# Performance work log

Hardware: AMD Instinct MI355X
Metric: run time of the kernel (lower is better)

Reference implementation:

```python
import jax, jax.numpy as jnp
import numpy as np
import math

D_MODEL = 512
N_HEADS = 16
HEAD_DIM = D_MODEL // N_HEADS  # 32
ROPE_BASE = 10000.0
B, T = 2, 2048


def build_rope_cache(seq_len, dim, base):
    inv_freq = 1.0 / (base ** (jnp.arange(0, dim, 2, dtype=jnp.float32) / dim))  # (dim/2,)
    t = jnp.arange(seq_len, dtype=jnp.float32)
    freqs = jnp.outer(t, inv_freq)                  # (T, dim/2)
    emb = jnp.concatenate([freqs, freqs], axis=-1)  # (T, dim)
    return jnp.cos(emb), jnp.sin(emb)


def rotate_half(x):
    x1, x2 = jnp.split(x, 2, axis=-1)
    return jnp.concatenate([-x2, x1], axis=-1)


def apply_rope(x, cos, sin):
    # x: (B,H,T,hd); cos/sin: (T,hd) broadcast over B,H
    return x * cos + rotate_half(x) * sin


def setup_inputs() -> dict:
    key = jax.random.key(0)
    k1, k2, k3 = jax.random.split(key, 3)
    x = jax.random.normal(k1, (B, T, D_MODEL), dtype=jnp.float32)
    w_qkv = jax.random.normal(k2, (3 * D_MODEL, D_MODEL), dtype=jnp.float32) * 0.02
    w_o = jax.random.normal(k3, (D_MODEL, D_MODEL), dtype=jnp.float32) * 0.02
    return {"x": x, "w_qkv": w_qkv, "w_o": w_o}


def reference(x, w_qkv, w_o):
    Bx, Tx, C = x.shape
    H, hd = N_HEADS, HEAD_DIM
    qkv = x @ w_qkv.T                                   # (B,T,3C)
    qkv = qkv.reshape(Bx, Tx, 3, H, hd).transpose(0, 2, 3, 1, 4)  # (B,3,H,T,hd)
    q, k, v = qkv[:, 0], qkv[:, 1], qkv[:, 2]
    cos, sin = build_rope_cache(Tx, hd, ROPE_BASE)
    q = apply_rope(q, cos, sin)
    k = apply_rope(k, cos, sin)
    scale = 1.0 / math.sqrt(hd)
    scores = jnp.einsum('bhqd,bhkd->bhqk', q, k) * scale  # (B,H,T,T)
    causal = jnp.tril(jnp.ones((Tx, Tx), dtype=bool))
    scores = jnp.where(causal, scores, jnp.finfo(scores.dtype).min)
    attn = jax.nn.softmax(scores, axis=-1)
    out = jnp.einsum('bhqk,bhkd->bhqd', attn, v)          # (B,H,T,hd)
    out = out.transpose(0, 2, 1, 3).reshape(Bx, Tx, C)    # (B,T,C)
    return out @ w_o.T
```

## Files before the change

kernel.cpp:

```cpp
#include <hip/hip_runtime.h>
#include <hip/hip_bf16.h>
#include <math.h>

#define D_MODEL 512
#define N_HEADS 16
#define HEAD_DIM 32
#define T_SEQ 2048
#define B_SZ 2
#define NTOK (B_SZ * T_SEQ)
#define QKV_DIM (3 * D_MODEL)

#define LOG2_10000_D16 0.8304820237218405f
#define QSCALE_LOG2 0.2550348788f
#define NROPE (T_SEQ * 16)

typedef short short8 __attribute__((ext_vector_type(8)));
typedef float f32x4  __attribute__((ext_vector_type(4)));

__device__ __forceinline__ float bf2f(unsigned int u16) {
    union { unsigned int i; float f; } v;
    v.i = u16 << 16;
    return v.f;
}

__device__ __forceinline__ unsigned short f2bf(float f) {
    union { float f; unsigned int i; } v;
    v.f = f;
    unsigned int lsb = (v.i >> 16) & 1u;
    v.i += 0x7fffu + lsb;
    return (unsigned short)(v.i >> 16);
}

__device__ __forceinline__ unsigned short f2bf_trunc(float f) {
    union { float f; unsigned int i; } v;
    v.f = f;
    return (unsigned short)(v.i >> 16);
}

__device__ __forceinline__ void gld_lds16(const void* g, void* l) {
    __builtin_amdgcn_global_load_lds(
        (const __attribute__((address_space(1))) void*)g,
        (__attribute__((address_space(3))) void*)l, 16, 0, 0);
}

#define N4_X   (NTOK * D_MODEL / 4)
#define N4_WQ  (QKV_DIM * D_MODEL / 4)
#define N4_WO  (D_MODEL * D_MODEL / 4)
__global__ __launch_bounds__(256) void cvt_all(const float* __restrict__ x,
                                               const float* __restrict__ wq,
                                               const float* __restrict__ wo,
                                               unsigned short* __restrict__ xb,
                                               unsigned short* __restrict__ wqb,
                                               unsigned short* __restrict__ wob,
                                               float2* __restrict__ rope) {
    int i = blockIdx.x * 256 + threadIdx.x;
    if (i >= N4_X + N4_WQ + N4_WO) {
        int kk = i - (N4_X + N4_WQ + N4_WO);
        if (kk < NROPE) {
            int t = kk >> 4, cd = kk & 15;
            float invf = exp2f(-LOG2_10000_D16 * (float)cd);
            float ss, cc;
            sincosf((float)t * invf, &ss, &cc);
            rope[kk] = make_float2(cc, ss);
        }
        return;
    }
    const float* in;
    unsigned short* out;
    int k;
    if (i < N4_X)                { in = x;  out = xb;  k = i; }
    else if (i < N4_X + N4_WQ)   { in = wq; out = wqb; k = i - N4_X; }
    else                         { in = wo; out = wob; k = i - N4_X - N4_WQ; }
    float4 v = ((const float4*)in)[k];
    ushort4 o;
    o.x = f2bf(v.x); o.y = f2bf(v.y); o.z = f2bf(v.z); o.w = f2bf(v.w);
    ((ushort4*)out)[k] = o;
}

template<int MT, int LDA, int LDC, bool OUT_BF16, bool ROPE>
__global__ __launch_bounds__(256) void gemm_nt(const unsigned short* __restrict__ A,
                                               const unsigned short* __restrict__ B,
                                               void* __restrict__ Cout,
                                               unsigned short* __restrict__ kb,
                                               unsigned short* __restrict__ vt,
                                               const float2* __restrict__ rope) {
    __shared__ unsigned short Als[MT * 64];
    __shared__ unsigned short Bls[64 * 64];

    const int tid = threadIdx.x;
    const int m0 = blockIdx.y * MT;
    const int n0 = blockIdx.x * 64;

    const int wid  = tid >> 6;
    const int lane = tid & 63;
    const int c    = lane & 15;
    const int quad = lane >> 4;
    const int wm = (wid >> 1) * (MT / 2);
    const int wn = (wid & 1) * 32;
    const int MI = MT / 32;

    f32x4 acc[MI][2];
#pragma unroll
    for (int i = 0; i < MI; ++i)
#pragma unroll
        for (int j = 0; j < 2; ++j) acc[i][j] = (f32x4)0.f;

    const int srow = wid * 8 + (lane >> 3);
    const int schk = lane & 7;

    for (int k0 = 0; k0 < 512; k0 += 64) {
#pragma unroll
        for (int it = 0; it < MT / 32; ++it) {
            const unsigned short* g = A + (size_t)(m0 + it * 32 + srow) * LDA + k0 + schk * 8;
            gld_lds16(g, &Als[(it * 32 + srow) * 64 + schk * 8]);
        }
#pragma unroll
        for (int it = 0; it < 2; ++it) {
            const unsigned short* g = B + (size_t)(n0 + it * 32 + srow) * 512 + k0 + schk * 8;
            gld_lds16(g, &Bls[(it * 32 + srow) * 64 + schk * 8]);
        }
        __syncthreads();

#pragma unroll
        for (int kk = 0; kk < 2; ++kk) {
            short8 af[MI], bfr[2];
#pragma unroll
            for (int i = 0; i < MI; ++i)
                af[i] = *(const short8*)&Als[(wm + i * 16 + c) * 64 + kk * 32 + quad * 8];
#pragma unroll
            for (int j = 0; j < 2; ++j)
                bfr[j] = *(const short8*)&Bls[(wn + j * 16 + c) * 64 + kk * 32 + quad * 8];
#pragma unroll
            for (int i = 0; i < MI; ++i)
#pragma unroll
                for (int j = 0; j < 2; ++j)
                    acc[i][j] = __builtin_amdgcn_mfma_f32_16x16x32_bf16(af[i], bfr[j], acc[i][j], 0, 0, 0);
        }
        __syncthreads();
    }

    if (ROPE) {
        const int sec = n0 >> 9;
        if (sec == 0) {
            const float2* rp = rope + c;
#pragma unroll
            for (int i = 0; i < MI; ++i)
#pragma unroll
                for (int r = 0; r < 4; ++r) {
                    int t = (m0 + wm + i * 16 + quad * 4 + r) & (T_SEQ - 1);
                    float2 cs = rp[t * 16];
                    float e0 = acc[i][0][r], e1 = acc[i][1][r];
                    acc[i][0][r] = (e0 * cs.x - e1 * cs.y) * QSCALE_LOG2;
                    acc[i][1][r] = (e1 * cs.x + e0 * cs.y) * QSCALE_LOG2;
                }
        } else if (sec == 1) {
            const float2* rp = rope + c;
            const int head = ((n0 - 512) + wn) >> 5;
#pragma unroll
            for (int i = 0; i < MI; ++i)
#pragma unroll
                for (int r = 0; r < 4; ++r) {
                    int mm = m0 + wm + i * 16 + quad * 4 + r;
                    int t = mm & (T_SEQ - 1);
                    float2 cs = rp[t * 16];
                    float e0 = acc[i][0][r], e1 = acc[i][1][r];
                    float k0v = e0 * cs.x - e1 * cs.y;
                    float k1v = e1 * cs.x + e0 * cs.y;
                    int bh = (mm >> 11) * 16 + head;
                    int s = (t & 3) ^ ((t >> 2) & 3);
                    unsigned short* row = kb + ((size_t)(bh * 2048 + t)) * 32;
                    row[((((c) >> 3) ^ s) << 3) + (c & 7)]        = f2bf(k0v);
                    row[((((16 + c) >> 3) ^ s) << 3) + (c & 7)]   = f2bf(k1v);
                }
            return;
        } else {
#pragma unroll
            for (int i = 0; i < MI; ++i)
#pragma unroll
                for (int j = 0; j < 2; ++j) {
                    int nl = n0 - 1024 + wn + j * 16;
                    int head = nl >> 5;
                    int d = (nl & 16) + c;
                    int mm = m0 + wm + i * 16 + quad * 4;
                    int bI = mm >> 11;
                    int pos = mm & (T_SEQ - 1);
                    int phys = ((pos >> 3) & 7) ^ (d & 7);
                    size_t base = ((size_t)((bI * 16 + head) * 32 + d)) * 2048
                                  + (pos & ~63) + (phys << 3) + (pos & 7);
                    ushort4 st;
                    st.x = f2bf(acc[i][j][0]); st.y = f2bf(acc[i][j][1]);
                    st.z = f2bf(acc[i][j][2]); st.w = f2bf(acc[i][j][3]);
                    *(ushort4*)(vt + base) = st;
                }
            return;
        }
    }

    if (OUT_BF16) {
        unsigned short* Cb = (unsigned short*)Cout;
#pragma unroll
        for (int i = 0; i < MI; ++i)
#pragma unroll
            for (int j = 0; j < 2; ++j)
#pragma unroll
                for (int r = 0; r < 4; ++r) {
                    int mm = m0 + wm + i * 16 + quad * 4 + r;
                    int nn = n0 + wn + j * 16 + c;
                    Cb[(size_t)mm * LDC + nn] = f2bf(acc[i][j][r]);
                }
    } else {
        float* Cf = (float*)Cout;
#pragma unroll
        for (int i = 0; i < MI; ++i)
#pragma unroll
            for (int j = 0; j < 2; ++j)
#pragma unroll
                for (int r = 0; r < 4; ++r) {
                    int mm = m0 + wm + i * 16 + quad * 4 + r;
                    int nn = n0 + wn + j * 16 + c;
                    Cf[(size_t)mm * LDC + nn] = acc[i][j][r];
                }
    }
}

__global__ __launch_bounds__(256) void flash_attn(unsigned short* __restrict__ qb,
                                                  const unsigned short* __restrict__ kb,
                                                  const unsigned short* __restrict__ vt) {
    __shared__ unsigned short KtL[2][64 * 32];
    __shared__ unsigned short VtL[2][32 * 64];
    __shared__ unsigned short Pl[4 * 16 * 64];

    const int idx   = blockIdx.x;
    const int qtile = 31 - (idx >> 5);
    const int bh    = idx & 31;
    const int b = bh >> 4, h = bh & 15;
    const int tid  = threadIdx.x;
    const int wid  = tid >> 6;
    const int lane = tid & 63;
    const int c    = lane & 15;
    const int quad = lane >> 4;

    const int q0w = qtile * 64 + wid * 16;
    const int sK = (c & 3) ^ ((c >> 2) & 3);
    const int sP = c & 7;

    short8 qf = *(const short8*)(qb + ((size_t)(b * T_SEQ + q0w + c)) * 512 + h * HEAD_DIM + quad * 8);

    f32x4 accO[2];
    accO[0] = (f32x4)0.f; accO[1] = (f32x4)0.f;
    float l_r[4] = {0.f, 0.f, 0.f, 0.f};

    unsigned short* plw = &Pl[wid * 16 * 64];

    const int krow = tid >> 2, kch = tid & 3;
    const int vd   = tid >> 3, vch = tid & 7;
    const unsigned short* kbase = kb + (size_t)bh * 2048 * 32 + (size_t)krow * 32 + kch * 8;
    const unsigned short* vbase = vt + ((size_t)(bh * 32 + vd)) * 2048 + vch * 8;

    uint4 kreg = *(const uint4*)(kbase);
    uint4 vreg = *(const uint4*)(vbase);
    *(uint4*)&KtL[0][tid * 8] = kreg;
    *(uint4*)&VtL[0][tid * 8] = vreg;
    __syncthreads();

    const int nkt = qtile + 1;
    for (int kt = 0; kt < nkt; ++kt) {
        const int cur = kt & 1;
        const bool pf_next = (kt + 1 < nkt);
        if (pf_next) {
            kreg = *(const uint4*)(kbase + (size_t)(kt + 1) * 64 * 32);
            vreg = *(const uint4*)(vbase + (size_t)(kt + 1) * 64);
        }

        f32x4 sv[4];
        __builtin_amdgcn_s_setprio(1);
#pragma unroll
        for (int j = 0; j < 4; ++j) {
            short8 kf = *(const short8*)&KtL[cur][(j * 16 + c) * 32 + ((quad ^ sK) << 3)];
            f32x4 z = (f32x4)0.f;
            sv[j] = __builtin_amdgcn_mfma_f32_16x16x32_bf16(qf, kf, z, 0, 0, 0);
        }
        __builtin_amdgcn_s_setprio(0);

        if (kt == qtile) {
#pragma unroll
            for (int j = 0; j < 4; ++j)
#pragma unroll
                for (int r = 0; r < 4; ++r)
                    if (j * 16 + c > wid * 16 + quad * 4 + r) sv[j][r] = -30000.f;
        }

#pragma unroll
        for (int j = 0; j < 4; ++j)
#pragma unroll
            for (int r = 0; r < 4; ++r) {
                float p = exp2f(sv[j][r]);
                l_r[r] += p;
                int row = quad * 4 + r;
                plw[row * 64 + (((j * 2 + (c >> 3)) ^ (row & 7)) << 3) + (c & 7)] = f2bf_trunc(p);
            }

        __builtin_amdgcn_s_setprio(1);
#pragma unroll
        for (int kk = 0; kk < 2; ++kk) {
            short8 pf = *(const short8*)&plw[c * 64 + (((kk * 4 + quad) ^ sP) << 3)];
#pragma unroll
            for (int ns = 0; ns < 2; ++ns) {
                short8 vf = *(const short8*)&VtL[cur][(ns * 16 + c) * 64 + (((kk * 4 + quad) ^ sP) << 3)];
                accO[ns] = __builtin_amdgcn_mfma_f32_16x16x32_bf16(pf, vf, accO[ns], 0, 0, 0);
            }
        }
        __builtin_amdgcn_s_setprio(0);

        if (pf_next) {
            *(uint4*)&KtL[cur ^ 1][tid * 8] = kreg;
            *(uint4*)&VtL[cur ^ 1][tid * 8] = vreg;
        }
        __syncthreads();
    }

#pragma unroll
    for (int r = 0; r < 4; ++r) {
        float lr = l_r[r];
        lr += __shfl_xor(lr, 1);
        lr += __shfl_xor(lr, 2);
        lr += __shfl_xor(lr, 4);
        lr += __shfl_xor(lr, 8);
        float inv = 1.f / lr;
        int qg = q0w + quad * 4 + r;
        unsigned short* op = qb + ((size_t)(b * T_SEQ + qg)) * 512 + h * HEAD_DIM;
#pragma unroll
        for (int ns = 0; ns < 2; ++ns)
            op[ns * 16 + c] = f2bf(accO[ns][r] * inv);
    }
}

extern "C" void kernel_launch(void* const* d_in, const int* in_sizes, int n_in,
                              void* d_out, int out_size, void* d_ws, size_t ws_size,
                              hipStream_t stream) {
    const float* x     = (const float*)d_in[0];
    const float* w_qkv = (const float*)d_in[1];
    const float* w_o   = (const float*)d_in[2];
    float* out = (float*)d_out;

    unsigned short* qb  = (unsigned short*)d_ws;
    unsigned short* kb  = qb  + (size_t)NTOK * D_MODEL;
    unsigned short* vt  = kb  + (size_t)32 * 2048 * 32;
    unsigned short* xb  = vt  + (size_t)32 * 32 * 2048;
    unsigned short* wqb = xb  + (size_t)NTOK * D_MODEL;
    unsigned short* wob = wqb + (size_t)QKV_DIM * D_MODEL;
    float2*         rope = (float2*)(wob + (size_t)D_MODEL * D_MODEL);

    {
        int total = N4_X + N4_WQ + N4_WO + NROPE;
        cvt_all<<<(total + 255) / 256, 256, 0, stream>>>(x, w_qkv, w_o, xb, wqb, wob, rope);
    }
    {
        dim3 grid(QKV_DIM / 64, NTOK / 128);
        gemm_nt<128, D_MODEL, D_MODEL, true, true><<<grid, 256, 0, stream>>>(xb, wqb, qb, kb, vt, rope);
    }
    {
        flash_attn<<<1024, 256, 0, stream>>>(qb, kb, vt);
    }
    {
        dim3 grid(D_MODEL / 64, NTOK / 64);
        gemm_nt<64, D_MODEL, D_MODEL, false, false><<<grid, 256, 0, stream>>>(qb, wob, out, nullptr, nullptr, nullptr);
    }
}
```

Measured before the change: 124.1 us.

## Split long causal query tiles across two blocks and combine partial outputs

The 16 longest causal query tiles per head now have their key range split between two blocks, which write unnormalized partial outputs and row sums to workspace. A new combine kernel adds the two partials, normalizes them, and writes bf16 results. Short tiles still run in a single block and write their output directly. The aim is to shorten the critical path caused by the triangular imbalance of work across blocks. The cost is an extra kernel launch plus fp32 partial-result traffic. Summing partials without rescaling is only correct because the kernel appears not to subtract a per-row running max.

```diff
diff --git a/kernel.cpp b/kernel.cpp
--- a/kernel.cpp
+++ b/kernel.cpp
@@ -225,14 +225,34 @@
 
 __global__ __launch_bounds__(256) void flash_attn(unsigned short* __restrict__ qb,
                                                   const unsigned short* __restrict__ kb,
-                                                  const unsigned short* __restrict__ vt) {
+                                                  const unsigned short* __restrict__ vt,
+                                                  float* __restrict__ pO,
+                                                  float* __restrict__ pL) {
     __shared__ unsigned short KtL[2][64 * 32];
     __shared__ unsigned short VtL[2][32 * 64];
     __shared__ unsigned short Pl[4 * 16 * 64];
 
-    const int idx   = blockIdx.x;
-    const int qtile = 31 - (idx >> 5);
-    const int bh    = idx & 31;
+    const int blk = blockIdx.x;
+    const int g   = blk >> 5;
+    const int bh  = blk & 31;
+    int qtile, kt0, ktN, sidx;
+    bool partial;
+    if (g < 16) {
+        qtile = 31 - g;
+        int nkt = qtile + 1;
+        kt0 = 0; ktN = nkt >> 1;
+        partial = true; sidx = (qtile - 16) * 2;
+    } else if (g < 32) {
+        qtile = 31 - (g - 16);
+        int nkt = qtile + 1;
+        kt0 = nkt >> 1; ktN = nkt;
+        partial = true; sidx = (qtile - 16) * 2 + 1;
+    } else {
+        qtile = 15 - (g - 32);
+        kt0 = 0; ktN = qtile + 1;
+        partial = false; sidx = 0;
+    }
+
     const int b = bh >> 4, h = bh & 15;
     const int tid  = threadIdx.x;
     const int wid  = tid >> 6;
@@ -257,16 +277,15 @@
     const unsigned short* kbase = kb + (size_t)bh * 2048 * 32 + (size_t)krow * 32 + kch * 8;
     const unsigned short* vbase = vt + ((size_t)(bh * 32 + vd)) * 2048 + vch * 8;
 
-    uint4 kreg = *(const uint4*)(kbase);
-    uint4 vreg = *(const uint4*)(vbase);
+    uint4 kreg = *(const uint4*)(kbase + (size_t)kt0 * 64 * 32);
+    uint4 vreg = *(const uint4*)(vbase + (size_t)kt0 * 64);
     *(uint4*)&KtL[0][tid * 8] = kreg;
     *(uint4*)&VtL[0][tid * 8] = vreg;
     __syncthreads();
 
-    const int nkt = qtile + 1;
-    for (int kt = 0; kt < nkt; ++kt) {
-        const int cur = kt & 1;
-        const bool pf_next = (kt + 1 < nkt);
+    for (int kt = kt0; kt < ktN; ++kt) {
+        const int cur = (kt - kt0) & 1;
+        const bool pf_next = (kt + 1 < ktN);
         if (pf_next) {
             kreg = *(const uint4*)(kbase + (size_t)(kt + 1) * 64 * 32);
             vreg = *(const uint4*)(vbase + (size_t)(kt + 1) * 64);
@@ -326,13 +345,45 @@
         lr += __shfl_xor(lr, 2);
         lr += __shfl_xor(lr, 4);
         lr += __shfl_xor(lr, 8);
-        float inv = 1.f / lr;
-        int qg = q0w + quad * 4 + r;
-        unsigned short* op = qb + ((size_t)(b * T_SEQ + qg)) * 512 + h * HEAD_DIM;
-#pragma unroll
-        for (int ns = 0; ns < 2; ++ns)
-            op[ns * 16 + c] = f2bf(accO[ns][r] * inv);
-    }
+        int qrl = wid * 16 + quad * 4 + r;
+        if (partial) {
+            size_t rb = ((size_t)(bh * 32 + sidx)) * 64 + qrl;
+            if (c == 0) pL[rb] = lr;
+            pO[rb * 32 + c]      = accO[0][r];
+            pO[rb * 32 + 16 + c] = accO[1][r];
+        } else {
+            float inv = 1.f / lr;
+            int qg = qtile * 64 + qrl;
+            unsigned short* op = qb + ((size_t)(b * T_SEQ + qg)) * 512 + h * HEAD_DIM;
+#pragma unroll
+            for (int ns = 0; ns < 2; ++ns)
+                op[ns * 16 + c] = f2bf(accO[ns][r] * inv);
+        }
+    }
+}
+
+__global__ __launch_bounds__(256) void combine_split(const float* __restrict__ pO,
+                                                     const float* __restrict__ pL,
+                                                     unsigned short* __restrict__ qb) {
+    int idx = blockIdx.x * 256 + threadIdx.x;
+    int row = idx >> 3;
+    int dc  = (idx & 7) * 4;
+    int bh  = row >> 10;
+    int rem = row & 1023;
+    int qt16 = rem >> 6;
+    int qr  = rem & 63;
+    size_t slot0 = ((size_t)(bh * 32 + qt16 * 2)) * 64 + qr;
+    float4 a  = *(const float4*)(pO + slot0 * 32 + dc);
+    float4 bv = *(const float4*)(pO + (slot0 + 64) * 32 + dc);
+    float inv = 1.f / (pL[slot0] + pL[slot0 + 64]);
+    ushort4 o;
+    o.x = f2bf((a.x + bv.x) * inv);
+    o.y = f2bf((a.y + bv.y) * inv);
+    o.z = f2bf((a.z + bv.z) * inv);
+    o.w = f2bf((a.w + bv.w) * inv);
+    int t = (16 + qt16) * 64 + qr;
+    int b = bh >> 4, h = bh & 15;
+    *(ushort4*)(qb + ((size_t)(b * T_SEQ + t)) * 512 + h * HEAD_DIM + dc) = o;
 }
 
 extern "C" void kernel_launch(void* const* d_in, const int* in_sizes, int n_in,
@@ -350,6 +401,8 @@
     unsigned short* wqb = xb  + (size_t)NTOK * D_MODEL;
     unsigned short* wob = wqb + (size_t)QKV_DIM * D_MODEL;
     float2*         rope = (float2*)(wob + (size_t)D_MODEL * D_MODEL);
+    float*          pO   = (float*)(rope + NROPE);
+    float*          pL   = pO + (size_t)32 * 32 * 64 * 32;
 
     {
         int total = N4_X + N4_WQ + N4_WO + NROPE;
@@ -360,7 +413,10 @@
         gemm_nt<128, D_MODEL, D_MODEL, true, true><<<grid, 256, 0, stream>>>(xb, wqb, qb, kb, vt, rope);
     }
     {
-        flash_attn<<<1024, 256, 0, stream>>>(qb, kb, vt);
+        flash_attn<<<1536, 256, 0, stream>>>(qb, kb, vt, pO, pL);
+    }
+    {
+        combine_split<<<262144 / 256, 256, 0, stream>>>(pO, pL, qb);
     }
     {
         dim3 grid(D_MODEL / 64, NTOK / 64);
```

New measurement: 125.8 us. No clear change (+1.4%).
